# Performance work log

Hardware: AMD Instinct MI355X
Metric: run time of the kernel (lower is better)

## Reference

```python
import jax, jax.numpy as jnp
import numpy as np

B, N, H = 4, 200, 300


def setup_inputs() -> dict:
    key = jax.random.key(0)
    ks = jax.random.split(key, 6)
    s = 1.0 / np.sqrt(H)
    return {
        "x": jax.random.normal(ks[0], (B, N, H), dtype=jnp.float32),
        "e": jax.random.normal(ks[1], (B, N, N, H), dtype=jnp.float32),
        "U_w": jax.random.uniform(ks[2], (H, H), jnp.float32, -s, s),
        "U_b": jax.random.uniform(ks[3], (H,), jnp.float32, -s, s),
        "V_w": jax.random.uniform(ks[4], (H, H), jnp.float32, -s, s),
        "V_b": jax.random.uniform(ks[5], (H,), jnp.float32, -s, s),
    }


def reference(x, e, U_w, U_b, V_w, V_b):
    # Ue = e @ U_w.T + U_b  -> (B, N, N, H)
    Ue = jnp.einsum("bijh,gh->bijg", e, U_w) + U_b
    # Vx = x @ V_w.T + V_b  -> (B, N, H)
    Vx = jnp.einsum("bnh,gh->bng", x, V_w) + V_b
    # e_new[b,i,j] = Ue[b,i,j] + Vx[b,i] + Vx[b,j]
    e_new = Ue + Vx[:, :, None, :] + Vx[:, None, :, :]
    return e_new
```

## Files before the change

kernel.cpp:

```cpp
#include <hip/hip_runtime.h>
#include <hip/hip_bf16.h>

#define BB 4
#define NN 200
#define HH 300
#define GF 20
#define BM 128
#define BCHUNK 40960

typedef __attribute__((ext_vector_type(8))) short short8;
typedef __attribute__((ext_vector_type(4))) float float4v;

static __device__ __forceinline__ ushort f2bf(float x) {
    union { float f; uint u; } v; v.f = x;
    uint r = v.u + 0x7FFFu + ((v.u >> 16) & 1u);
    return (ushort)(r >> 16);
}

static __device__ __forceinline__ short8 pack8_cvt(float4v a, float4v b) {
    uint u0, u1, u2, u3;
    asm("v_cvt_pk_bf16_f32 %0, %1, %2" : "=v"(u0) : "v"(a[0]), "v"(a[1]));
    asm("v_cvt_pk_bf16_f32 %0, %1, %2" : "=v"(u1) : "v"(a[2]), "v"(a[3]));
    asm("v_cvt_pk_bf16_f32 %0, %1, %2" : "=v"(u2) : "v"(b[0]), "v"(b[1]));
    asm("v_cvt_pk_bf16_f32 %0, %1, %2" : "=v"(u3) : "v"(b[2]), "v"(b[3]));
    union { uint u[4]; short8 s; } r;
    r.u[0] = u0; r.u[1] = u1; r.u[2] = u2; r.u[3] = u3;
    return r.s;
}

static __device__ __forceinline__ void gload_lds16(const void* g, void* l) {
    __builtin_amdgcn_global_load_lds(
        (const __attribute__((address_space(1))) unsigned int*)g,
        (__attribute__((address_space(3))) unsigned int*)l, 16, 0, 0);
}

__global__ void pack_u(const float* __restrict__ Uw, ushort* __restrict__ Bp) {
    int idx = blockIdx.x * 256 + threadIdx.x;
    if (idx >= 10 * GF * 64) return;
    int lane = idx & 63;
    int kg = idx >> 6;
    int gf = kg % GF, ks = kg / GF;
    int g = gf * 16 + (lane & 15);
    int h0 = ks * 32 + (lane >> 4) * 8;
    ushort v[8];
#pragma unroll
    for (int j = 0; j < 8; ++j) {
        int h = h0 + j;
        v[j] = (g < HH && h < HH) ? f2bf(Uw[g * HH + h]) : (ushort)0;
    }
    *reinterpret_cast<short8*>(Bp + (size_t)idx * 8) = *reinterpret_cast<const short8*>(v);
}

__global__ void vx_kernel(const float* __restrict__ x, const float* __restrict__ Vw,
                          const float* __restrict__ Vb, const float* __restrict__ Ub,
                          float* __restrict__ Vx) {
    __shared__ float xs[HH];
    int row = blockIdx.x;
    const float* xr = x + (size_t)row * HH;
    for (int h = threadIdx.x; h < HH; h += 256) xs[h] = xr[h];
    __syncthreads();
    for (int g = threadIdx.x; g < HH; g += 256) {
        const float4* wr = reinterpret_cast<const float4*>(Vw + (size_t)g * HH);
        const float4* xv = reinterpret_cast<const float4*>(xs);
        float s0 = 0.f, s1 = 0.f, s2 = 0.f, s3 = 0.f;
#pragma unroll 5
        for (int k = 0; k < HH / 4; ++k) {
            float4 w = wr[k];
            float4 xx = xv[k];
            s0 += w.x * xx.x; s1 += w.y * xx.y; s2 += w.z * xx.z; s3 += w.w * xx.w;
        }
        Vx[(size_t)row * HH + g] = Vb[g] + 0.5f * Ub[g] + s0 + s1 + s2 + s3;
    }
}

__launch_bounds__(512, 2)
__global__ void gemm_kernel(const float* __restrict__ e, const ushort* __restrict__ Bp,
                            const float* __restrict__ Vx, float* __restrict__ out) {
    __shared__ __align__(16) char SMEM[147456];
    const int tid = threadIdx.x;
    const int w = tid >> 6, l = tid & 63;
    const int r = l & 15, q = l >> 4;
    const int m0 = blockIdx.x * BM;

#define AFB(P_) (SMEM + (P_) * 32768)
#define BFB(P_) (SMEM + 65536 + (P_) * 40960)

#define WAITV(N_) asm volatile("s_waitcnt vmcnt(" #N_ ")" ::: "memory")
#define BAR() do {                                                   \
        __builtin_amdgcn_sched_barrier(0);                           \
        asm volatile("s_waitcnt lgkmcnt(0)" ::: "memory");           \
        __builtin_amdgcn_sched_barrier(0);                           \
        __builtin_amdgcn_s_barrier();                                \
        __builtin_amdgcn_sched_barrier(0);                           \
    } while (0)

#define STAGE_A(KC_, P_) do {                                                   \
        _Pragma("unroll")                                                       \
        for (int rd_ = 0; rd_ < 4; ++rd_) {                                     \
            int row_ = rd_ * 32 + w * 4 + (l >> 4);                             \
            int ucl_ = (l & 15) ^ (row_ & 15);                                  \
            const char* src_ = (const char*)(e + (size_t)(m0 + row_) * HH)      \
                               + (KC_) * 256 + ucl_ * 16;                       \
            if ((KC_) == 4 && ucl_ >= 11) src_ = (const char*)e;                \
            gload_lds16(src_, AFB(P_) + rd_ * 8192 + w * 1024 + l * 16);        \
        }                                                                       \
    } while (0)

#define STAGE_B(KC_, P_) do {                                                   \
        const char* bs_ = (const char*)Bp + (size_t)(KC_) * BCHUNK;             \
        char* bd_ = BFB(P_);                                                    \
        _Pragma("unroll")                                                       \
        for (int rd_ = 0; rd_ < 5; ++rd_)                                       \
            gload_lds16(bs_ + rd_ * 8192 + tid * 16, bd_ + rd_ * 8192 + tid * 16); \
    } while (0)

    float4v acc[GF];
#pragma unroll
    for (int f = 0; f < GF; ++f) acc[f] = (float4v){0.f, 0.f, 0.f, 0.f};

#define COMPUTE(P_) do {                                                        \
        const char* ab_ = AFB(P_) + (w * 16 + r) * 256;                         \
        const ushort* bb_ = (const ushort*)BFB(P_);                             \
        _Pragma("unroll")                                                       \
        for (int s_ = 0; s_ < 2; ++s_) {                                        \
            int u0_ = (s_ * 8 + 2 * q) ^ r;                                     \
            int u1_ = (s_ * 8 + 2 * q + 1) ^ r;                                 \
            float4v fa0_ = *reinterpret_cast<const float4v*>(ab_ + u0_ * 16);   \
            float4v fa1_ = *reinterpret_cast<const float4v*>(ab_ + u1_ * 16);   \
            short8 fa_ = pack8_cvt(fa0_, fa1_);                                 \
            const ushort* bs_ = bb_ + s_ * (GF * 512) + l * 8;                  \
            _Pragma("unroll")                                                   \
            for (int f_ = 0; f_ < GF; ++f_) {                                   \
                short8 bfr_ = *reinterpret_cast<const short8*>(bs_ + f_ * 512); \
                acc[f_] = __builtin_amdgcn_mfma_f32_16x16x32_bf16(bfr_, fa_, acc[f_], 0, 0, 0); \
            }                                                                   \
        }                                                                       \
    } while (0)

    STAGE_A(0, 0); STAGE_B(0, 0);
    STAGE_A(1, 1); STAGE_B(1, 1);
    WAITV(9); BAR();

    COMPUTE(0); BAR();
    STAGE_A(2, 0); STAGE_B(2, 0); WAITV(9); BAR();

    COMPUTE(1); BAR();
    STAGE_A(3, 1); STAGE_B(3, 1); WAITV(9); BAR();

    COMPUTE(0); BAR();
    STAGE_A(4, 0); STAGE_B(4, 0); WAITV(9); BAR();

    COMPUTE(1); BAR();
    WAITV(0); BAR();

    COMPUTE(0);

    asm volatile("s_waitcnt lgkmcnt(0)" ::: "memory");
    __builtin_amdgcn_s_barrier();
    __builtin_amdgcn_sched_barrier(0);

    char* ep = SMEM + w * 10496;
    const int mbase = m0 + w * 16;

#pragma unroll
    for (int gh2 = 0; gh2 < 2; ++gh2) {
        if (gh2) {
            asm volatile("s_waitcnt lgkmcnt(0)" ::: "memory");
            __builtin_amdgcn_sched_barrier(0);
        }
#pragma unroll
        for (int ff = 0; ff < 10; ++ff) {
            int f = gh2 * 10 + ff;
            if (f < 19)
                *reinterpret_cast<float4v*>(ep + r * 656 + ff * 64 + q * 16) = acc[f];
        }
        asm volatile("s_waitcnt lgkmcnt(0)" ::: "memory");
        __builtin_amdgcn_sched_barrier(0);
        const int nl = gh2 ? 35 : 40;
#pragma unroll 4
        for (int rr = 0; rr < 16; ++rr) {
            if (l < nl) {
                float4v v = *reinterpret_cast<const float4v*>(ep + rr * 656 + l * 16);
                int m = mbase + rr;
                int j = m % NN;
                int ti = m / NN;
                int b = ti / NN;
                int g0 = gh2 * 160 + l * 4;
                float4v vi4 = *reinterpret_cast<const float4v*>(Vx + (size_t)ti * HH + g0);
                float4v vj4 = *reinterpret_cast<const float4v*>(Vx + (size_t)(b * NN + j) * HH + g0);
                *reinterpret_cast<float4v*>(out + (size_t)m * HH + g0) = v + vi4 + vj4;
            }
        }
    }
#undef COMPUTE
#undef STAGE_A
#undef STAGE_B
#undef BAR
#undef WAITV
#undef AFB
#undef BFB
}

extern "C" void kernel_launch(void* const* d_in, const int* in_sizes, int n_in,
                              void* d_out, int out_size, void* d_ws, size_t ws_size,
                              hipStream_t stream) {
    const float* x  = (const float*)d_in[0];
    const float* e  = (const float*)d_in[1];
    const float* Uw = (const float*)d_in[2];
    const float* Ub = (const float*)d_in[3];
    const float* Vw = (const float*)d_in[4];
    const float* Vb = (const float*)d_in[5];
    float* out = (float*)d_out;

    ushort* Bp = (ushort*)d_ws;
    float*  Vx = (float*)((char*)d_ws + 204800);

    pack_u<<<50, 256, 0, stream>>>(Uw, Bp);
    vx_kernel<<<BB * NN, 256, 0, stream>>>(x, Vw, Vb, Ub, Vx);
    gemm_kernel<<<160000 / BM, 512, 0, stream>>>(e, Bp, Vx, out);
}
```

Measured before the change: 149.9 us.

## Pre-convert e to bf16 MFMA tiles and split GEMM over output halves

Adds a pack_e pre-pass that converts the large fp32 edge tensor into bf16, laid out in fragment order. A new gemm2 kernel then stages those tiles directly into LDS and splits each 128-row tile into two blocks, one per half of the output features. The aim is to take the in-loop fp32-to-bf16 conversion and swizzled LDS access out of the GEMM and to raise occupancy through smaller LDS buffers. The cost is an extra full write and read of a ~100MB intermediate, plus A tiles that are re-read by both halves. The new path runs only when the workspace is large enough; otherwise it falls back to the old kernel.

```diff
diff --git a/kernel.cpp b/kernel.cpp
--- a/kernel.cpp
+++ b/kernel.cpp
@@ -4,9 +4,15 @@
 #define BB 4
 #define NN 200
 #define HH 300
+#define NCH 10
 #define GF 20
-#define BM 128
-#define BCHUNK 40960
+#define GHF 10
+#define NTILE 5000
+#define WS_BP    0
+#define WS_BPF   204800
+#define WS_VX    409600
+#define WS_EBF   1369600
+#define WS_NEED  (WS_EBF + 102400000ull)
 
 typedef __attribute__((ext_vector_type(8))) short short8;
 typedef __attribute__((ext_vector_type(4))) float float4v;
@@ -34,9 +40,28 @@
         (__attribute__((address_space(3))) unsigned int*)l, 16, 0, 0);
 }
 
-__global__ void pack_u(const float* __restrict__ Uw, ushort* __restrict__ Bp) {
+__global__ void pack_u_gh(const float* __restrict__ Uw, ushort* __restrict__ Bp) {
     int idx = blockIdx.x * 256 + threadIdx.x;
-    if (idx >= 10 * GF * 64) return;
+    if (idx >= 2 * NCH * GHF * 64) return;
+    int lane = idx & 63;
+    int rem = idx >> 6;
+    int fh = rem % GHF;
+    int ks = (rem / GHF) % NCH;
+    int gh = rem / (GHF * NCH);
+    int g = (gh * GHF + fh) * 16 + (lane & 15);
+    int h0 = ks * 32 + (lane >> 4) * 8;
+    ushort v[8];
+#pragma unroll
+    for (int j = 0; j < 8; ++j) {
+        int h = h0 + j;
+        v[j] = (g < HH && h < HH) ? f2bf(Uw[g * HH + h]) : (ushort)0;
+    }
+    *reinterpret_cast<short8*>(Bp + (size_t)idx * 8) = *reinterpret_cast<const short8*>(v);
+}
+
+__global__ void pack_u_full(const float* __restrict__ Uw, ushort* __restrict__ Bp) {
+    int idx = blockIdx.x * 256 + threadIdx.x;
+    if (idx >= NCH * GF * 64) return;
     int lane = idx & 63;
     int kg = idx >> 6;
     int gf = kg % GF, ks = kg / GF;
@@ -73,18 +98,142 @@
     }
 }
 
+__global__ void pack_e(const float* __restrict__ e, ushort* __restrict__ ebf) {
+    int id = blockIdx.x * 256 + threadIdx.x;
+    int lane = id & 63;
+    int rem = id >> 6;
+    int half = rem & 1;
+    int tks = rem >> 1;
+    int ks = tks % NCH;
+    int t = tks / NCH;
+    int r = lane & 15, q = lane >> 4;
+    int row = t * 32 + half * 16 + r;
+    int c0 = ks * 32 + q * 8;
+    const float* rp = e + (size_t)row * HH;
+    const float* p0 = (c0 + 4 <= HH) ? rp + c0 : e;
+    const float* p1 = (c0 + 8 <= HH) ? rp + c0 + 4 : e;
+    float4v a = *reinterpret_cast<const float4v*>(p0);
+    float4v b = *reinterpret_cast<const float4v*>(p1);
+    short8 w = pack8_cvt(a, b);
+    if (ks == NCH - 1) {
+#pragma unroll
+        for (int j = 0; j < 8; ++j)
+            if (c0 + j >= HH) w[j] = 0;
+    }
+    *reinterpret_cast<short8*>(ebf + (size_t)id * 8) = w;
+}
+
 __launch_bounds__(512, 2)
-__global__ void gemm_kernel(const float* __restrict__ e, const ushort* __restrict__ Bp,
-                            const float* __restrict__ Vx, float* __restrict__ out) {
+__global__ void gemm2(const ushort* __restrict__ ebf, const ushort* __restrict__ Bp,
+                      const float* __restrict__ Vx, float* __restrict__ out) {
+    __shared__ __align__(16) ushort Aa[2][8192];
+    __shared__ __align__(16) ushort Bb[2][10240];
+    const int tid = threadIdx.x;
+    const int w = tid >> 6, l = tid & 63;
+    const int r = l & 15, q = l >> 4;
+    const int gh = blockIdx.x & 1;
+    const int mb = blockIdx.x >> 1;
+    const int m0 = mb * 128;
+    const int t0 = mb * 4;
+    const char* bbase = (const char*)Bp + (size_t)gh * 102400;
+
+    float4v acc[GHF];
+#pragma unroll
+    for (int f = 0; f < GHF; ++f) acc[f] = (float4v){0.f, 0.f, 0.f, 0.f};
+
+#define STAGE_A(KC_, P_) do {                                                   \
+        _Pragma("unroll")                                                       \
+        for (int rd_ = 0; rd_ < 2; ++rd_) {                                     \
+            int tile_ = t0 + rd_ * 2 + (tid >> 8);                              \
+            const char* src_ = (const char*)ebf                                 \
+                + ((size_t)(tile_ * NCH + 2 * (KC_)) * 2048) + (tid & 255) * 16;\
+            gload_lds16(src_, (char*)&Aa[P_][0] + rd_ * 8192 + tid * 16);       \
+        }                                                                       \
+    } while (0)
+
+#define STAGE_B(KC_, P_) do {                                                   \
+        const char* bs_ = bbase + (size_t)(KC_) * 20480;                        \
+        char* bd_ = (char*)&Bb[P_][0];                                          \
+        gload_lds16(bs_ + tid * 16,        bd_ + tid * 16);                     \
+        gload_lds16(bs_ + 8192 + tid * 16, bd_ + 8192 + tid * 16);              \
+        if (tid < 256)                                                          \
+            gload_lds16(bs_ + 16384 + tid * 16, bd_ + 16384 + tid * 16);        \
+    } while (0)
+
+#define COMPUTE(P_) do {                                                        \
+        const char* ab_ = (const char*)&Aa[P_][0] + (w >> 1) * 4096 + (w & 1) * 1024; \
+        const char* bb_ = (const char*)&Bb[P_][0];                              \
+        _Pragma("unroll")                                                       \
+        for (int ki_ = 0; ki_ < 2; ++ki_) {                                     \
+            short8 fa_ = *reinterpret_cast<const short8*>(ab_ + ki_ * 2048 + l * 16); \
+            const char* bk_ = bb_ + ki_ * 10240 + l * 16;                       \
+            _Pragma("unroll")                                                   \
+            for (int f_ = 0; f_ < GHF; ++f_) {                                  \
+                short8 bf_ = *reinterpret_cast<const short8*>(bk_ + f_ * 1024); \
+                acc[f_] = __builtin_amdgcn_mfma_f32_16x16x32_bf16(bf_, fa_, acc[f_], 0, 0, 0); \
+            }                                                                   \
+        }                                                                       \
+    } while (0)
+
+#define WAITV(N_) do {                                                          \
+        __builtin_amdgcn_sched_barrier(0);                                      \
+        asm volatile("s_waitcnt vmcnt(" #N_ ")" ::: "memory");                  \
+        __builtin_amdgcn_sched_barrier(0);                                      \
+    } while (0)
+
+#define BAR() do {                                                              \
+        asm volatile("s_waitcnt lgkmcnt(0)" ::: "memory");                      \
+        __builtin_amdgcn_s_barrier();                                           \
+        __builtin_amdgcn_sched_barrier(0);                                      \
+    } while (0)
+
+    STAGE_A(0, 0); STAGE_B(0, 0);
+    STAGE_A(1, 1); STAGE_B(1, 1);
+    WAITV(4); BAR();
+
+    COMPUTE(0); BAR(); STAGE_A(2, 0); STAGE_B(2, 0); WAITV(4); BAR();
+    COMPUTE(1); BAR(); STAGE_A(3, 1); STAGE_B(3, 1); WAITV(4); BAR();
+    COMPUTE(0); BAR(); STAGE_A(4, 0); STAGE_B(4, 0); WAITV(4); BAR();
+    COMPUTE(1); BAR(); WAITV(0); BAR();
+    COMPUTE(0);
+
+    {
+        const int m = m0 + (w >> 1) * 32 + (w & 1) * 16 + r;
+        int j = m % NN;
+        int ti = m / NN;
+        int b = ti / NN;
+        const float* vi = Vx + (size_t)ti * HH;
+        const float* vj = Vx + (size_t)(b * NN + j) * HH;
+        float* orow = out + (size_t)m * HH;
+        const int gb = gh * (GHF * 16);
+#pragma unroll
+        for (int f = 0; f < GHF; ++f) {
+            int g0 = gb + f * 16 + q * 4;
+            if (g0 + 4 <= HH) {
+                float4v vi4 = *reinterpret_cast<const float4v*>(vi + g0);
+                float4v vj4 = *reinterpret_cast<const float4v*>(vj + g0);
+                *reinterpret_cast<float4v*>(orow + g0) = acc[f] + vi4 + vj4;
+            }
+        }
+    }
+#undef STAGE_A
+#undef STAGE_B
+#undef COMPUTE
+#undef WAITV
+#undef BAR
+}
+
+__launch_bounds__(512, 2)
+__global__ void gemm_fb(const float* __restrict__ e, const ushort* __restrict__ Bp,
+                        const float* __restrict__ Vx, float* __restrict__ out) {
     __shared__ __align__(16) char SMEM[147456];
     const int tid = threadIdx.x;
     const int w = tid >> 6, l = tid & 63;
     const int r = l & 15, q = l >> 4;
-    const int m0 = blockIdx.x * BM;
+    const int m0 = blockIdx.x * 128;
 
 #define AFB(P_) (SMEM + (P_) * 32768)
 #define BFB(P_) (SMEM + 65536 + (P_) * 40960)
-
 #define WAITV(N_) asm volatile("s_waitcnt vmcnt(" #N_ ")" ::: "memory")
 #define BAR() do {                                                   \
         __builtin_amdgcn_sched_barrier(0);                           \
@@ -93,7 +242,6 @@
         __builtin_amdgcn_s_barrier();                                \
         __builtin_amdgcn_sched_barrier(0);                           \
     } while (0)
-
 #define STAGE_A(KC_, P_) do {                                                   \
         _Pragma("unroll")                                                       \
         for (int rd_ = 0; rd_ < 4; ++rd_) {                                     \
@@ -105,9 +253,8 @@
             gload_lds16(src_, AFB(P_) + rd_ * 8192 + w * 1024 + l * 16);        \
         }                                                                       \
     } while (0)
-
 #define STAGE_B(KC_, P_) do {                                                   \
-        const char* bs_ = (const char*)Bp + (size_t)(KC_) * BCHUNK;             \
+        const char* bs_ = (const char*)Bp + (size_t)(KC_) * 40960;              \
         char* bd_ = BFB(P_);                                                    \
         _Pragma("unroll")                                                       \
         for (int rd_ = 0; rd_ < 5; ++rd_)                                       \
@@ -140,34 +287,20 @@
     STAGE_A(0, 0); STAGE_B(0, 0);
     STAGE_A(1, 1); STAGE_B(1, 1);
     WAITV(9); BAR();
-
-    COMPUTE(0); BAR();
-    STAGE_A(2, 0); STAGE_B(2, 0); WAITV(9); BAR();
-
-    COMPUTE(1); BAR();
-    STAGE_A(3, 1); STAGE_B(3, 1); WAITV(9); BAR();
-
-    COMPUTE(0); BAR();
-    STAGE_A(4, 0); STAGE_B(4, 0); WAITV(9); BAR();
-
-    COMPUTE(1); BAR();
-    WAITV(0); BAR();
-
+    COMPUTE(0); BAR(); STAGE_A(2, 0); STAGE_B(2, 0); WAITV(9); BAR();
+    COMPUTE(1); BAR(); STAGE_A(3, 1); STAGE_B(3, 1); WAITV(9); BAR();
+    COMPUTE(0); BAR(); STAGE_A(4, 0); STAGE_B(4, 0); WAITV(9); BAR();
+    COMPUTE(1); BAR(); WAITV(0); BAR();
     COMPUTE(0);
 
     asm volatile("s_waitcnt lgkmcnt(0)" ::: "memory");
     __builtin_amdgcn_s_barrier();
     __builtin_amdgcn_sched_barrier(0);
-
     char* ep = SMEM + w * 10496;
     const int mbase = m0 + w * 16;
-
 #pragma unroll
     for (int gh2 = 0; gh2 < 2; ++gh2) {
-        if (gh2) {
-            asm volatile("s_waitcnt lgkmcnt(0)" ::: "memory");
-            __builtin_amdgcn_sched_barrier(0);
-        }
+        if (gh2) { asm volatile("s_waitcnt lgkmcnt(0)" ::: "memory"); __builtin_amdgcn_sched_barrier(0); }
 #pragma unroll
         for (int ff = 0; ff < 10; ++ff) {
             int f = gh2 * 10 + ff;
@@ -212,10 +345,19 @@
     const float* Vb = (const float*)d_in[5];
     float* out = (float*)d_out;
 
-    ushort* Bp = (ushort*)d_ws;
-    float*  Vx = (float*)((char*)d_ws + 204800);
-
-    pack_u<<<50, 256, 0, stream>>>(Uw, Bp);
+    ushort* Bp  = (ushort*)((char*)d_ws + WS_BP);
+    ushort* BpF = (ushort*)((char*)d_ws + WS_BPF);
+    float*  Vx  = (float*)((char*)d_ws + WS_VX);
+    ushort* ebf = (ushort*)((char*)d_ws + WS_EBF);
+
     vx_kernel<<<BB * NN, 256, 0, stream>>>(x, Vw, Vb, Ub, Vx);
-    gemm_kernel<<<160000 / BM, 512, 0, stream>>>(e, Bp, Vx, out);
-}
+
+    if (ws_size >= WS_NEED) {
+        pack_u_gh<<<50, 256, 0, stream>>>(Uw, Bp);
+        pack_e<<<25000, 256, 0, stream>>>(e, ebf);
+        gemm2<<<2500, 512, 0, stream>>>(ebf, Bp, Vx, out);
+    } else {
+        pack_u_full<<<50, 256, 0, stream>>>(Uw, BpF);
+        gemm_fb<<<1250, 512, 0, stream>>>(e, BpF, Vx, out);
+    }
+}
```

Result: slower. 204.8 us (+36.6%).
